# Performance work log

Measured on AMD Instinct MI355X. Metric: run time of the kernel, lower is better.

The kernel has to match this reference:

```python
import jax, jax.numpy as jnp
import numpy as np

GAMMA = 0.99
CLIP_VALUE = 5.0
B, T = 4096, 2048


def setup_inputs() -> dict:
    key = jax.random.key(0)
    k1, k2, k3, k4 = jax.random.split(key, 4)
    return {
        "log_probs": jax.random.normal(k1, (B, T), dtype=jnp.float32),
        "logits": jax.random.normal(k2, (B, T, 1), dtype=jnp.float32),
        "weight": jax.random.uniform(k3, (B, T), dtype=jnp.float32),
        "baselines": jax.random.normal(k4, (B, T, 1), dtype=jnp.float32),
    }


def _discounted_cumulative(wr, gamma):
    # wr: [B, T]. cum[t] = sum_{s>=t} gamma^(s-t) * wr[s]
    # Reverse-time linear recurrence: c[t] = wr[t] + gamma * c[t+1]
    def step(c, x):
        c = x + gamma * c
        return c, c
    # scan over time in reverse; xs laid out time-major [T, B]
    _, cum_rev = jax.lax.scan(step, jnp.zeros(wr.shape[0], wr.dtype), wr[:, ::-1].T)
    return cum_rev[::-1].T  # back to [B, T]


def reference(log_probs, logits, weight, baselines):
    rewards = jax.nn.log_sigmoid(logits[..., 0])          # [B, T]
    cumulative_rewards = _discounted_cumulative(weight * rewards, GAMMA)  # [B, T]
    advantages = cumulative_rewards - baselines[..., 0]
    advantages = advantages - advantages.mean(axis=0)      # center over batch
    advantages = jnp.clip(advantages, -CLIP_VALUE, CLIP_VALUE)
    generator_objective = (advantages * log_probs).sum(axis=0)  # [T]
    return (generator_objective, cumulative_rewards)
```

## Files before the change

### kernel.cpp

```cpp
#include <hip/hip_runtime.h>
#include <math.h>

#define BDIM 4096
#define TDIM 2048

constexpr double gpow(int e) {
    double r = 1.0;
    for (int i = 0; i < e; ++i) r *= 0.99;
    return r;
}

__device__ __forceinline__ float logsig(float x) {
    return fminf(x, 0.0f) - log1pf(expf(-fabsf(x)));
}

__global__ __launch_bounds__(256, 4) void k1_scan(
    const float* __restrict__ logits,
    const float* __restrict__ weight,
    const float* __restrict__ baselines,
    float* __restrict__ cum_out,
    float* __restrict__ partial,
    int rows_per_block)
{
    const int tid  = threadIdx.x;
    const int lane = tid & 63;
    const int wave = tid >> 6;
    const int t0   = tid * 8;

    const float G    = 0.99f;
    const float G8   = (float)gpow(8);
    const float G512 = (float)gpow(512);
    const float LOG2G = -0.014499569695115089f;
    const float gk[8] = {(float)gpow(8), (float)gpow(7), (float)gpow(6), (float)gpow(5),
                         (float)gpow(4), (float)gpow(3), (float)gpow(2), (float)gpow(1)};

    const float lane_pow = exp2f((float)((64 - lane) * 8) * LOG2G);

    __shared__ float wsum[2][4];

    float colacc[8];
#pragma unroll
    for (int k = 0; k < 8; ++k) colacc[k] = 0.0f;

    const int row0 = blockIdx.x * rows_per_block;
    size_t base = (size_t)row0 * TDIM + t0;

    float4 x0 = *reinterpret_cast<const float4*>(logits + base);
    float4 x1 = *reinterpret_cast<const float4*>(logits + base + 4);
    float4 w0 = *reinterpret_cast<const float4*>(weight + base);
    float4 w1 = *reinterpret_cast<const float4*>(weight + base + 4);
    float4 b0 = *reinterpret_cast<const float4*>(baselines + base);
    float4 b1 = *reinterpret_cast<const float4*>(baselines + base + 4);

    for (int r = 0; r < rows_per_block; ++r) {
        const size_t nbase = base + TDIM;
        const bool has_next = (r + 1 < rows_per_block);

        float wr[8];
        wr[0] = w0.x * logsig(x0.x); wr[1] = w0.y * logsig(x0.y);
        wr[2] = w0.z * logsig(x0.z); wr[3] = w0.w * logsig(x0.w);
        wr[4] = w1.x * logsig(x1.x); wr[5] = w1.y * logsig(x1.y);
        wr[6] = w1.z * logsig(x1.z); wr[7] = w1.w * logsig(x1.w);

        float4 nx0, nx1, nw0, nw1, nb0, nb1;
        if (has_next) {
            nx0 = *reinterpret_cast<const float4*>(logits + nbase);
            nx1 = *reinterpret_cast<const float4*>(logits + nbase + 4);
            nw0 = *reinterpret_cast<const float4*>(weight + nbase);
            nw1 = *reinterpret_cast<const float4*>(weight + nbase + 4);
            nb0 = *reinterpret_cast<const float4*>(baselines + nbase);
            nb1 = *reinterpret_cast<const float4*>(baselines + nbase + 4);
        }

        float loc[8];
        loc[7] = wr[7];
#pragma unroll
        for (int k = 6; k >= 0; --k) loc[k] = fmaf(G, loc[k + 1], wr[k]);

        float v = loc[0];
        float f = G8;
#pragma unroll
        for (int o = 1; o < 64; o <<= 1) {
            float up = __shfl_down(v, (unsigned)o, 64);
            if (lane + o < 64) v = fmaf(f, up, v);
            f *= f;
        }

        const int buf = r & 1;
        if (lane == 0) wsum[buf][wave] = v;
        __syncthreads();
        const float W1 = wsum[buf][1], W2 = wsum[buf][2], W3 = wsum[buf][3];
        const float FC3 = W3;
        const float FC2 = fmaf(G512, FC3, W2);
        const float FC1 = fmaf(G512, FC2, W1);
        const float carry = (wave == 0) ? FC1 : (wave == 1) ? FC2 : (wave == 2) ? FC3 : 0.0f;

        const float vfull = fmaf(lane_pow, carry, v);
        const float vn = __shfl_down(vfull, 1, 64);
        const float tail = (lane == 63) ? carry : vn;

        float c[8];
#pragma unroll
        for (int k = 0; k < 8; ++k) c[k] = fmaf(gk[k], tail, loc[k]);

        *reinterpret_cast<float4*>(cum_out + base)     = make_float4(c[0], c[1], c[2], c[3]);
        *reinterpret_cast<float4*>(cum_out + base + 4) = make_float4(c[4], c[5], c[6], c[7]);

        colacc[0] += c[0] - b0.x; colacc[1] += c[1] - b0.y;
        colacc[2] += c[2] - b0.z; colacc[3] += c[3] - b0.w;
        colacc[4] += c[4] - b1.x; colacc[5] += c[5] - b1.y;
        colacc[6] += c[6] - b1.z; colacc[7] += c[7] - b1.w;

        base = nbase;
        if (has_next) {
            x0 = nx0; x1 = nx1; w0 = nw0; w1 = nw1; b0 = nb0; b1 = nb1;
        }
    }

    const size_t pbase = (size_t)blockIdx.x * TDIM + t0;
    *reinterpret_cast<float4*>(partial + pbase)     = make_float4(colacc[0], colacc[1], colacc[2], colacc[3]);
    *reinterpret_cast<float4*>(partial + pbase + 4) = make_float4(colacc[4], colacc[5], colacc[6], colacc[7]);
}

__global__ __launch_bounds__(256) void k2_colsum(
    const float* __restrict__ partial, float* __restrict__ colsum, int rows_per_slice)
{
    const int gid   = blockIdx.x * 256 + threadIdx.x;
    const int col   = gid & (TDIM - 1);
    const int slice = gid >> 11;
    const float* p = partial + (size_t)slice * rows_per_slice * TDIM + col;
    float s = 0.0f;
#pragma unroll 8
    for (int i = 0; i < rows_per_slice; ++i) s += p[(size_t)i * TDIM];
    atomicAdd(colsum + col, s);
}

#define K3_ROWS 16
__global__ __launch_bounds__(256) void k3_obj(
    const float* __restrict__ cum,
    const float* __restrict__ baselines,
    const float* __restrict__ lp,
    const float* __restrict__ colsum,
    float* __restrict__ obj)
{
    const int c4 = (blockIdx.x * 256 + threadIdx.x) * 4;
    const int r0 = blockIdx.y * K3_ROWS;
    const float inv = 1.0f / (float)BDIM;
    float4 ms = *reinterpret_cast<const float4*>(colsum + c4);
    const float m0 = ms.x * inv, m1 = ms.y * inv, m2 = ms.z * inv, m3 = ms.w * inv;

    float a0 = 0.0f, a1 = 0.0f, a2 = 0.0f, a3 = 0.0f;
    size_t idx = (size_t)r0 * TDIM + c4;
#pragma unroll 4
    for (int r = 0; r < K3_ROWS; ++r, idx += TDIM) {
        float4 c = *reinterpret_cast<const float4*>(cum + idx);
        float4 b = *reinterpret_cast<const float4*>(baselines + idx);
        float4 l = *reinterpret_cast<const float4*>(lp + idx);
        float v0 = fminf(fmaxf(c.x - b.x - m0, -5.0f), 5.0f);
        float v1 = fminf(fmaxf(c.y - b.y - m1, -5.0f), 5.0f);
        float v2 = fminf(fmaxf(c.z - b.z - m2, -5.0f), 5.0f);
        float v3 = fminf(fmaxf(c.w - b.w - m3, -5.0f), 5.0f);
        a0 = fmaf(v0, l.x, a0);
        a1 = fmaf(v1, l.y, a1);
        a2 = fmaf(v2, l.z, a2);
        a3 = fmaf(v3, l.w, a3);
    }
    atomicAdd(obj + c4 + 0, a0);
    atomicAdd(obj + c4 + 1, a1);
    atomicAdd(obj + c4 + 2, a2);
    atomicAdd(obj + c4 + 3, a3);
}

extern "C" void kernel_launch(void* const* d_in, const int* in_sizes, int n_in,
                              void* d_out, int out_size, void* d_ws, size_t ws_size,
                              hipStream_t stream) {
    const float* log_probs = (const float*)d_in[0];
    const float* logits    = (const float*)d_in[1];
    const float* weight    = (const float*)d_in[2];
    const float* baselines = (const float*)d_in[3];

    float* out = (float*)d_out;
    float* obj = out;
    float* cum = out + TDIM;

    const size_t need1024 = ((size_t)1024 * TDIM + TDIM) * sizeof(float);
    const int rpb = (ws_size >= need1024) ? 4 : 8;
    const int k1_blocks = BDIM / rpb;

    float* partial = (float*)d_ws;
    float* colsum  = partial + (size_t)k1_blocks * TDIM;

    hipMemsetAsync(obj, 0, TDIM * sizeof(float), stream);
    hipMemsetAsync(colsum, 0, TDIM * sizeof(float), stream);

    k1_scan<<<k1_blocks, 256, 0, stream>>>(logits, weight, baselines, cum, partial, rpb);
    k2_colsum<<<256, 256, 0, stream>>>(partial, colsum, k1_blocks / 32);
    k3_obj<<<dim3(TDIM / (256 * 4), BDIM / K3_ROWS), 256, 0, stream>>>(
        cum, baselines, log_probs, colsum, obj);
}
```

Before: 202.3 us.

## Fold memsets into scan kernel, fast logsigmoid, fix rows-per-block, retile objective

Drops the two hipMemsetAsync calls and zeroes colsum and obj from blocks 0 and 1 of the scan kernel instead. It switches log-sigmoid to the fast __expf/__logf intrinsics, fixes rows per block at 8 (512 blocks), and precomputes the shuffle-scan gamma powers. The objective kernel now does 32 rows per block to halve its atomics. Fewer blocks in the scan means fewer waves in flight, and the fast intrinsics trade some accuracy for speed.

```diff
diff --git a/kernel.cpp b/kernel.cpp
--- a/kernel.cpp
+++ b/kernel.cpp
@@ -3,6 +3,8 @@
 
 #define BDIM 4096
 #define TDIM 2048
+#define NBLK 512
+#define RPB  8
 
 constexpr double gpow(int e) {
     double r = 1.0;
@@ -10,30 +12,45 @@
     return r;
 }
 
-__device__ __forceinline__ float logsig(float x) {
-    return fminf(x, 0.0f) - log1pf(expf(-fabsf(x)));
-}
-
-__global__ __launch_bounds__(256, 4) void k1_scan(
+__device__ __forceinline__ float logsig_fast(float x) {
+    float z = __expf(-fabsf(x));
+    return fminf(x, 0.0f) - __logf(1.0f + z);
+}
+
+__device__ __forceinline__ float clip5(float x) {
+    return fminf(fmaxf(x, -5.0f), 5.0f);
+}
+
+__global__ __launch_bounds__(256) void k1_scan(
     const float* __restrict__ logits,
     const float* __restrict__ weight,
     const float* __restrict__ baselines,
     float* __restrict__ cum_out,
     float* __restrict__ partial,
-    int rows_per_block)
+    float* __restrict__ colsum,
+    float* __restrict__ obj)
 {
     const int tid  = threadIdx.x;
     const int lane = tid & 63;
     const int wave = tid >> 6;
     const int t0   = tid * 8;
 
+    if (blockIdx.x == 0) {
+        *reinterpret_cast<float4*>(colsum + t0)     = make_float4(0.f, 0.f, 0.f, 0.f);
+        *reinterpret_cast<float4*>(colsum + t0 + 4) = make_float4(0.f, 0.f, 0.f, 0.f);
+    }
+    if (blockIdx.x == 1) {
+        *reinterpret_cast<float4*>(obj + t0)     = make_float4(0.f, 0.f, 0.f, 0.f);
+        *reinterpret_cast<float4*>(obj + t0 + 4) = make_float4(0.f, 0.f, 0.f, 0.f);
+    }
+
     const float G    = 0.99f;
-    const float G8   = (float)gpow(8);
     const float G512 = (float)gpow(512);
     const float LOG2G = -0.014499569695115089f;
     const float gk[8] = {(float)gpow(8), (float)gpow(7), (float)gpow(6), (float)gpow(5),
                          (float)gpow(4), (float)gpow(3), (float)gpow(2), (float)gpow(1)};
-
+    const float fs[6] = {(float)gpow(8),  (float)gpow(16), (float)gpow(32),
+                         (float)gpow(64), (float)gpow(128), (float)gpow(256)};
     const float lane_pow = exp2f((float)((64 - lane) * 8) * LOG2G);
 
     __shared__ float wsum[2][4];
@@ -42,7 +59,7 @@
 #pragma unroll
     for (int k = 0; k < 8; ++k) colacc[k] = 0.0f;
 
-    const int row0 = blockIdx.x * rows_per_block;
+    const int row0 = blockIdx.x * RPB;
     size_t base = (size_t)row0 * TDIM + t0;
 
     float4 x0 = *reinterpret_cast<const float4*>(logits + base);
@@ -52,15 +69,15 @@
     float4 b0 = *reinterpret_cast<const float4*>(baselines + base);
     float4 b1 = *reinterpret_cast<const float4*>(baselines + base + 4);
 
-    for (int r = 0; r < rows_per_block; ++r) {
+    for (int r = 0; r < RPB; ++r) {
         const size_t nbase = base + TDIM;
-        const bool has_next = (r + 1 < rows_per_block);
+        const bool has_next = (r + 1 < RPB);
 
         float wr[8];
-        wr[0] = w0.x * logsig(x0.x); wr[1] = w0.y * logsig(x0.y);
-        wr[2] = w0.z * logsig(x0.z); wr[3] = w0.w * logsig(x0.w);
-        wr[4] = w1.x * logsig(x1.x); wr[5] = w1.y * logsig(x1.y);
-        wr[6] = w1.z * logsig(x1.z); wr[7] = w1.w * logsig(x1.w);
+        wr[0] = w0.x * logsig_fast(x0.x); wr[1] = w0.y * logsig_fast(x0.y);
+        wr[2] = w0.z * logsig_fast(x0.z); wr[3] = w0.w * logsig_fast(x0.w);
+        wr[4] = w1.x * logsig_fast(x1.x); wr[5] = w1.y * logsig_fast(x1.y);
+        wr[6] = w1.z * logsig_fast(x1.z); wr[7] = w1.w * logsig_fast(x1.w);
 
         float4 nx0, nx1, nw0, nw1, nb0, nb1;
         if (has_next) {
@@ -78,12 +95,11 @@
         for (int k = 6; k >= 0; --k) loc[k] = fmaf(G, loc[k + 1], wr[k]);
 
         float v = loc[0];
-        float f = G8;
-#pragma unroll
-        for (int o = 1; o < 64; o <<= 1) {
+#pragma unroll
+        for (int s = 0; s < 6; ++s) {
+            const int o = 1 << s;
             float up = __shfl_down(v, (unsigned)o, 64);
-            if (lane + o < 64) v = fmaf(f, up, v);
-            f *= f;
+            if (lane + o < 64) v = fmaf(fs[s], up, v);
         }
 
         const int buf = r & 1;
@@ -123,19 +139,19 @@
 }
 
 __global__ __launch_bounds__(256) void k2_colsum(
-    const float* __restrict__ partial, float* __restrict__ colsum, int rows_per_slice)
+    const float* __restrict__ partial, float* __restrict__ colsum)
 {
-    const int gid   = blockIdx.x * 256 + threadIdx.x;
-    const int col   = gid & (TDIM - 1);
-    const int slice = gid >> 11;
-    const float* p = partial + (size_t)slice * rows_per_slice * TDIM + col;
+    const int gid = blockIdx.x * 256 + threadIdx.x;
+    const int col = gid & (TDIM - 1);
+    const int slc = gid >> 11;
+    const float* p = partial + (size_t)slc * 16 * TDIM + col;
     float s = 0.0f;
-#pragma unroll 8
-    for (int i = 0; i < rows_per_slice; ++i) s += p[(size_t)i * TDIM];
+#pragma unroll
+    for (int i = 0; i < 16; ++i) s += p[(size_t)i * TDIM];
     atomicAdd(colsum + col, s);
 }
 
-#define K3_ROWS 16
+#define K3_ROWS 32
 __global__ __launch_bounds__(256) void k3_obj(
     const float* __restrict__ cum,
     const float* __restrict__ baselines,
@@ -151,19 +167,15 @@
 
     float a0 = 0.0f, a1 = 0.0f, a2 = 0.0f, a3 = 0.0f;
     size_t idx = (size_t)r0 * TDIM + c4;
-#pragma unroll 4
+#pragma unroll 8
     for (int r = 0; r < K3_ROWS; ++r, idx += TDIM) {
         float4 c = *reinterpret_cast<const float4*>(cum + idx);
         float4 b = *reinterpret_cast<const float4*>(baselines + idx);
         float4 l = *reinterpret_cast<const float4*>(lp + idx);
-        float v0 = fminf(fmaxf(c.x - b.x - m0, -5.0f), 5.0f);
-        float v1 = fminf(fmaxf(c.y - b.y - m1, -5.0f), 5.0f);
-        float v2 = fminf(fmaxf(c.z - b.z - m2, -5.0f), 5.0f);
-        float v3 = fminf(fmaxf(c.w - b.w - m3, -5.0f), 5.0f);
-        a0 = fmaf(v0, l.x, a0);
-        a1 = fmaf(v1, l.y, a1);
-        a2 = fmaf(v2, l.z, a2);
-        a3 = fmaf(v3, l.w, a3);
+        a0 = fmaf(clip5(c.x - b.x - m0), l.x, a0);
+        a1 = fmaf(clip5(c.y - b.y - m1), l.y, a1);
+        a2 = fmaf(clip5(c.z - b.z - m2), l.z, a2);
+        a3 = fmaf(clip5(c.w - b.w - m3), l.w, a3);
     }
     atomicAdd(obj + c4 + 0, a0);
     atomicAdd(obj + c4 + 1, a1);
@@ -183,18 +195,11 @@
     float* obj = out;
     float* cum = out + TDIM;
 
-    const size_t need1024 = ((size_t)1024 * TDIM + TDIM) * sizeof(float);
-    const int rpb = (ws_size >= need1024) ? 4 : 8;
-    const int k1_blocks = BDIM / rpb;
-
     float* partial = (float*)d_ws;
-    float* colsum  = partial + (size_t)k1_blocks * TDIM;
-
-    hipMemsetAsync(obj, 0, TDIM * sizeof(float), stream);
-    hipMemsetAsync(colsum, 0, TDIM * sizeof(float), stream);
-
-    k1_scan<<<k1_blocks, 256, 0, stream>>>(logits, weight, baselines, cum, partial, rpb);
-    k2_colsum<<<256, 256, 0, stream>>>(partial, colsum, k1_blocks / 32);
+    float* colsum  = partial + (size_t)NBLK * TDIM;
+
+    k1_scan<<<NBLK, 256, 0, stream>>>(logits, weight, baselines, cum, partial, colsum, obj);
+    k2_colsum<<<256, 256, 0, stream>>>(partial, colsum);
     k3_obj<<<dim3(TDIM / (256 * 4), BDIM / K3_ROWS), 256, 0, stream>>>(
         cum, baselines, log_probs, colsum, obj);
 }
```

New measurement: 181.7 us. 10.1% less time.
